# Kernel tuning notes

Hardware: AMD Instinct MI355X
Metric: run time of the kernel (lower is better)

The kernel has to match this reference:

```python
import jax, jax.numpy as jnp
import numpy as np
from jax import lax

WINDOW_SIZE = 11
SIGMA = 1.5
CHANNEL = 1
DATA_RANGE = 1.0
C1 = (0.01 * DATA_RANGE) ** 2
C2 = (0.03 * DATA_RANGE) ** 2


def _gaussian_window(size, sigma, channel):
    coords = jnp.arange(size, dtype=jnp.float32) - size // 2
    g = jnp.exp(-coords ** 2 / (2.0 * sigma ** 2))
    g = g / g.sum()
    w2d = g[:, None] * g[None, :]                    # (size, size)
    # depthwise weight layout OIHW: (channel, 1, size, size)
    return jnp.broadcast_to(w2d[None, None], (channel, 1, size, size))


def setup_inputs() -> dict:
    key = jax.random.key(0)
    k1, k2 = jax.random.split(key)
    B, C, H, W = 64, CHANNEL, 512, 512
    x = jax.random.uniform(k1, (B, C, H, W), dtype=jnp.float32)
    y = jax.random.uniform(k2, (B, C, H, W), dtype=jnp.float32)
    window = _gaussian_window(WINDOW_SIZE, SIGMA, CHANNEL)
    return {"x": x, "y": y, "window": window}


def _apply_window(t, window):
    pad = WINDOW_SIZE // 2
    return lax.conv_general_dilated(
        t, window,
        window_strides=(1, 1),
        padding=((pad, pad), (pad, pad)),
        dimension_numbers=("NCHW", "OIHW", "NCHW"),
        feature_group_count=CHANNEL,
    )


def reference(x, y, window):
    mu_x = _apply_window(x, window)
    mu_y = _apply_window(y, window)
    mu_x_sq = mu_x ** 2
    mu_y_sq = mu_y ** 2
    mu_xy = mu_x * mu_y
    sigma_x_sq = _apply_window(x * x, window) - mu_x_sq
    sigma_y_sq = _apply_window(y * y, window) - mu_y_sq
    sigma_xy = _apply_window(x * y, window) - mu_xy
    numerator = (2.0 * mu_xy + C1) * (2.0 * sigma_xy + C2)
    denominator = (mu_x_sq + mu_y_sq + C1) * (sigma_x_sq + sigma_y_sq + C2)
    ssim_map = numerator / denominator
    ssim_per_sample = ssim_map.mean(axis=(1, 2, 3))
    return ssim_per_sample.mean()  # reduction='mean'
```

## Files before the change

### kernel.cpp

```cpp
#include <hip/hip_runtime.h>


#define IMG 512
#define BH 64
#define CHUNK 8
#define NCHUNK (BH / CHUNK)
#define SROW 522
#define NTHREADS 512

typedef __attribute__((ext_vector_type(2))) float f32x2;

static __device__ __forceinline__ f32x2 pk_fma(f32x2 a, f32x2 b, f32x2 c) {
    f32x2 d;
    asm("v_pk_fma_f32 %0, %1, %2, %3" : "=v"(d) : "v"(a), "v"(b), "v"(c));
    return d;
}
static __device__ __forceinline__ f32x2 pk_mul(f32x2 a, f32x2 b) {
    f32x2 d;
    asm("v_pk_mul_f32 %0, %1, %2" : "=v"(d) : "v"(a), "v"(b));
    return d;
}

__global__ __launch_bounds__(NTHREADS, 4) void ssim_band(
    const float* __restrict__ x, const float* __restrict__ y,
    const float* __restrict__ win, float* __restrict__ partial)
{
    __shared__ __align__(16) f32x2 vab[CHUNK][SROW];
    __shared__ __align__(16) f32x2 vqq[CHUNK][SROW];
    __shared__ float sg[11];
    __shared__ float redbuf[NTHREADS / 64];

    const int tid = threadIdx.x;

    if (tid < 11) {
        float s = 0.f;
        #pragma unroll
        for (int j = 0; j < 11; ++j) s += win[tid * 11 + j];
        sg[tid] = s;
    }
    if (tid < 160) {
        int plane = tid / 80, rem = tid % 80, row = rem / 10, pc = rem % 10;
        int cc = (pc < 5) ? pc : (512 + pc);
        f32x2 z = (f32x2)(0.f);
        if (plane == 0) vab[row][cc] = z; else vqq[row][cc] = z;
    }

    const int y0 = blockIdx.x * BH;
    const size_t img_off = (size_t)blockIdx.y * (IMG * IMG);
    const float* __restrict__ xb = x + img_off + tid;
    const float* __restrict__ yb = y + img_off + tid;

    f32x2 pab[18];
    #pragma unroll
    for (int j = 0; j < 10; ++j) {
        int gy = y0 - 5 + j;
        float a = 0.f, b = 0.f;
        if (gy >= 0) { a = xb[gy * IMG]; b = yb[gy * IMG]; }
        pab[j][0] = a + b;
        pab[j][1] = a - b;
    }

    __syncthreads();
    f32x2 g2[11];
    #pragma unroll
    for (int k = 0; k < 11; ++k) { float gv = sg[k]; g2[k][0] = gv; g2[k][1] = gv; }

    const float C1 = 1.0e-4f;
    const float C2 = 9.0e-4f;
    float acc = 0.f;

    const int rr = tid & 7;
    const int c0 = (tid >> 3) * 8;

    for (int k = 0; k < NCHUNK; ++k) {
        const int r0 = y0 + k * CHUNK;

        #pragma unroll
        for (int j = 0; j < 8; ++j) {
            int gy = r0 + 5 + j;
            float a = 0.f, b = 0.f;
            if (gy < IMG) { a = xb[gy * IMG]; b = yb[gy * IMG]; }
            pab[10 + j][0] = a + b;
            pab[10 + j][1] = a - b;
        }

        f32x2 sq[18];
        #pragma unroll
        for (int j = 0; j < 18; ++j) sq[j] = pk_mul(pab[j], pab[j]);

        #pragma unroll
        for (int i = 0; i < CHUNK; ++i) {
            f32x2 a = (f32x2)(0.f), q = (f32x2)(0.f);
            #pragma unroll
            for (int t = 0; t < 11; ++t) {
                a = pk_fma(g2[t], pab[i + t], a);
                q = pk_fma(g2[t], sq[i + t], q);
            }
            vab[i][tid + 5] = a;
            vqq[i][tid + 5] = q;
        }

        __syncthreads();

        {
            f32x2 mu[8], qq[8];
            {
                f32x2 t[18];
                const float4* p = (const float4*)&vab[rr][c0];
                #pragma unroll
                for (int q8 = 0; q8 < 9; ++q8) {
                    float4 f = p[q8];
                    t[2*q8][0] = f.x;  t[2*q8][1] = f.y;
                    t[2*q8+1][0] = f.z;  t[2*q8+1][1] = f.w;
                }
                #pragma unroll
                for (int i = 0; i < 8; ++i) {
                    f32x2 a = (f32x2)(0.f);
                    #pragma unroll
                    for (int t1 = 0; t1 < 11; ++t1) a = pk_fma(g2[t1], t[i + t1], a);
                    mu[i] = a;
                }
            }
            {
                f32x2 t[18];
                const float4* p = (const float4*)&vqq[rr][c0];
                #pragma unroll
                for (int q8 = 0; q8 < 9; ++q8) {
                    float4 f = p[q8];
                    t[2*q8][0] = f.x;  t[2*q8][1] = f.y;
                    t[2*q8+1][0] = f.z;  t[2*q8+1][1] = f.w;
                }
                #pragma unroll
                for (int i = 0; i < 8; ++i) {
                    f32x2 a = (f32x2)(0.f);
                    #pragma unroll
                    for (int t1 = 0; t1 < 11; ++t1) a = pk_fma(g2[t1], t[i + t1], a);
                    qq[i] = a;
                }
            }

            #pragma unroll
            for (int i = 0; i < 8; ++i) {
                f32x2 m2 = pk_mul(mu[i], mu[i]);
                float P = m2[0] + m2[1];
                float Q = m2[0] - m2[1];
                float R = qq[i][0] + qq[i][1];
                float S = qq[i][0] - qq[i][1];
                float num1 = fmaf(0.5f, Q, C1);
                float num2 = fmaf(0.5f, S - Q, C2);
                float den1 = fmaf(0.5f, P, C1);
                float den2 = fmaf(0.5f, R - P, C2);
                acc += (num1 * num2) * __builtin_amdgcn_rcpf(den1 * den2);
            }
        }

        __syncthreads();

        #pragma unroll
        for (int j = 0; j < 10; ++j) pab[j] = pab[j + 8];
    }

    #pragma unroll
    for (int off = 32; off > 0; off >>= 1) acc += __shfl_down(acc, off, 64);
    int wid = tid >> 6, lane = tid & 63;
    if (lane == 0) redbuf[wid] = acc;
    __syncthreads();
    if (tid == 0) {
        float ssum = 0.f;
        #pragma unroll
        for (int w = 0; w < NTHREADS / 64; ++w) ssum += redbuf[w];
        partial[blockIdx.y * gridDim.x + blockIdx.x] = ssum;
    }
}

#define NPART 512

__global__ __launch_bounds__(512) void ssim_finalize(
    const float* __restrict__ partial, float* __restrict__ out)
{
    __shared__ double red[8];
    double acc = (double)partial[threadIdx.x];
    #pragma unroll
    for (int off = 32; off > 0; off >>= 1) acc += __shfl_down(acc, off, 64);
    int wid = threadIdx.x >> 6, lane = threadIdx.x & 63;
    if (lane == 0) red[wid] = acc;
    __syncthreads();
    if (threadIdx.x == 0) {
        double ssum = 0.0;
        #pragma unroll
        for (int w = 0; w < 8; ++w) ssum += red[w];
        out[0] = (float)(ssum / (64.0 * 512.0 * 512.0));
    }
}

extern "C" void kernel_launch(void* const* d_in, const int* in_sizes, int n_in,
                              void* d_out, int out_size, void* d_ws, size_t ws_size,
                              hipStream_t stream) {
    (void)in_sizes; (void)n_in; (void)out_size; (void)ws_size;
    const float* x   = (const float*)d_in[0];
    const float* y   = (const float*)d_in[1];
    const float* win = (const float*)d_in[2];
    float* out = (float*)d_out;
    float* partial = (float*)d_ws;

    dim3 grid(IMG / BH, 64);
    ssim_band<<<grid, NTHREADS, 0, stream>>>(x, y, win, partial);
    ssim_finalize<<<1, NPART, 0, stream>>>(partial, out);
}
```

Baseline: 165.8 us.

## Software-pipeline global row loads and use LDS-only barriers

Loads the first 18 rows up front and prefetches the next chunk's 8 rows of x and y into registers while the current chunk is convolved, so global-load latency overlaps with compute. Block barriers now wait only on LDS counters rather than all memory, which lets the prefetched global loads stay in flight across the barrier. The trailing barrier is skipped on the last chunk. The LDS row stride is padded from 522 to 537 to change bank mapping, with the horizontal pass reading 8-byte elements instead of float4. In exchange, register pressure rises from the prefetch buffers, and the odd stride breaks the 16-byte alignment the float4 reads relied on.

```diff
diff --git a/kernel.cpp b/kernel.cpp
--- a/kernel.cpp
+++ b/kernel.cpp
@@ -5,8 +5,9 @@
 #define BH 64
 #define CHUNK 8
 #define NCHUNK (BH / CHUNK)
-#define SROW 522
+#define SROW 537
 #define NTHREADS 512
+#define GRIDX (IMG / BH)
 
 typedef __attribute__((ext_vector_type(2))) float f32x2;
 
@@ -19,6 +20,12 @@
     f32x2 d;
     asm("v_pk_mul_f32 %0, %1, %2" : "=v"(d) : "v"(a), "v"(b));
     return d;
+}
+
+static __device__ __forceinline__ void block_sync_lgkm() {
+    asm volatile("s_waitcnt lgkmcnt(0)" ::: "memory");
+    __builtin_amdgcn_s_barrier();
+    asm volatile("" ::: "memory");
 }
 
 __global__ __launch_bounds__(NTHREADS, 4) void ssim_band(
@@ -52,7 +59,7 @@
 
     f32x2 pab[18];
     #pragma unroll
-    for (int j = 0; j < 10; ++j) {
+    for (int j = 0; j < 18; ++j) {
         int gy = y0 - 5 + j;
         float a = 0.f, b = 0.f;
         if (gy >= 0) { a = xb[gy * IMG]; b = yb[gy * IMG]; }
@@ -60,7 +67,15 @@
         pab[j][1] = a - b;
     }
 
-    __syncthreads();
+    float pfa[8], pfb[8];
+    #pragma unroll
+    for (int j = 0; j < 8; ++j) {
+        int gy = y0 + 13 + j;
+        pfa[j] = 0.f; pfb[j] = 0.f;
+        if (gy < IMG) { pfa[j] = xb[gy * IMG]; pfb[j] = yb[gy * IMG]; }
+    }
+
+    block_sync_lgkm();
     f32x2 g2[11];
     #pragma unroll
     for (int k = 0; k < 11; ++k) { float gv = sg[k]; g2[k][0] = gv; g2[k][1] = gv; }
@@ -72,16 +87,25 @@
     const int rr = tid & 7;
     const int c0 = (tid >> 3) * 8;
 
+    #pragma unroll 1
     for (int k = 0; k < NCHUNK; ++k) {
-        const int r0 = y0 + k * CHUNK;
-
-        #pragma unroll
-        for (int j = 0; j < 8; ++j) {
-            int gy = r0 + 5 + j;
-            float a = 0.f, b = 0.f;
-            if (gy < IMG) { a = xb[gy * IMG]; b = yb[gy * IMG]; }
-            pab[10 + j][0] = a + b;
-            pab[10 + j][1] = a - b;
+        if (k) {
+            #pragma unroll
+            for (int j = 0; j < 10; ++j) pab[j] = pab[j + 8];
+            #pragma unroll
+            for (int j = 0; j < 8; ++j) {
+                pab[10 + j][0] = pfa[j] + pfb[j];
+                pab[10 + j][1] = pfa[j] - pfb[j];
+            }
+        }
+        if (k < NCHUNK - 1) {
+            int rbase = y0 + 8 * k + 13;
+            #pragma unroll
+            for (int j = 0; j < 8; ++j) {
+                int gy = rbase + j;
+                pfa[j] = 0.f; pfb[j] = 0.f;
+                if (gy < IMG) { pfa[j] = xb[gy * IMG]; pfb[j] = yb[gy * IMG]; }
+            }
         }
 
         f32x2 sq[18];
@@ -100,19 +124,15 @@
             vqq[i][tid + 5] = q;
         }
 
-        __syncthreads();
+        block_sync_lgkm();
 
         {
-            f32x2 mu[8], qq[8];
+            f32x2 mu[8], qq8[8];
             {
+                const f32x2* p = &vab[rr][c0];
                 f32x2 t[18];
-                const float4* p = (const float4*)&vab[rr][c0];
-                #pragma unroll
-                for (int q8 = 0; q8 < 9; ++q8) {
-                    float4 f = p[q8];
-                    t[2*q8][0] = f.x;  t[2*q8][1] = f.y;
-                    t[2*q8+1][0] = f.z;  t[2*q8+1][1] = f.w;
-                }
+                #pragma unroll
+                for (int i = 0; i < 18; ++i) t[i] = p[i];
                 #pragma unroll
                 for (int i = 0; i < 8; ++i) {
                     f32x2 a = (f32x2)(0.f);
@@ -122,20 +142,16 @@
                 }
             }
             {
+                const f32x2* p = &vqq[rr][c0];
                 f32x2 t[18];
-                const float4* p = (const float4*)&vqq[rr][c0];
-                #pragma unroll
-                for (int q8 = 0; q8 < 9; ++q8) {
-                    float4 f = p[q8];
-                    t[2*q8][0] = f.x;  t[2*q8][1] = f.y;
-                    t[2*q8+1][0] = f.z;  t[2*q8+1][1] = f.w;
-                }
+                #pragma unroll
+                for (int i = 0; i < 18; ++i) t[i] = p[i];
                 #pragma unroll
                 for (int i = 0; i < 8; ++i) {
                     f32x2 a = (f32x2)(0.f);
                     #pragma unroll
                     for (int t1 = 0; t1 < 11; ++t1) a = pk_fma(g2[t1], t[i + t1], a);
-                    qq[i] = a;
+                    qq8[i] = a;
                 }
             }
 
@@ -144,8 +160,8 @@
                 f32x2 m2 = pk_mul(mu[i], mu[i]);
                 float P = m2[0] + m2[1];
                 float Q = m2[0] - m2[1];
-                float R = qq[i][0] + qq[i][1];
-                float S = qq[i][0] - qq[i][1];
+                float R = qq8[i][0] + qq8[i][1];
+                float S = qq8[i][0] - qq8[i][1];
                 float num1 = fmaf(0.5f, Q, C1);
                 float num2 = fmaf(0.5f, S - Q, C2);
                 float den1 = fmaf(0.5f, P, C1);
@@ -154,10 +170,7 @@
             }
         }
 
-        __syncthreads();
-
-        #pragma unroll
-        for (int j = 0; j < 10; ++j) pab[j] = pab[j + 8];
+        if (k < NCHUNK - 1) block_sync_lgkm();
     }
 
     #pragma unroll
@@ -172,8 +185,6 @@
         partial[blockIdx.y * gridDim.x + blockIdx.x] = ssum;
     }
 }
-
-#define NPART 512
 
 __global__ __launch_bounds__(512) void ssim_finalize(
     const float* __restrict__ partial, float* __restrict__ out)
@@ -203,7 +214,7 @@
     float* out = (float*)d_out;
     float* partial = (float*)d_ws;
 
-    dim3 grid(IMG / BH, 64);
+    dim3 grid(GRIDX, 64);
     ssim_band<<<grid, NTHREADS, 0, stream>>>(x, y, win, partial);
-    ssim_finalize<<<1, NPART, 0, stream>>>(partial, out);
-}
+    ssim_finalize<<<1, 512, 0, stream>>>(partial, out);
+}
```

Measured after the change: 238.3 us. 1.44x slower.
